# Kernel optimization log

Measured on AMD Instinct MI355X. Metric: run time of the kernel, lower is better.

The kernel has to match this reference:

```python
import jax, jax.numpy as jnp
import numpy as np

B, T, C, H = 2, 2048, 1024, 16
HD = C // H  # head dim = 64


def setup_inputs() -> dict:
    key = jax.random.key(0)
    k1, k2, k3 = jax.random.split(key, 3)
    scale = 0.02
    x = jax.random.normal(k1, (B, T, C), dtype=jnp.float32)
    w_attn = jax.random.normal(k2, (C, 3 * C), dtype=jnp.float32) * scale
    b_attn = jnp.zeros((3 * C,), dtype=jnp.float32)
    w_proj = jax.random.normal(k3, (C, C), dtype=jnp.float32) * scale
    b_proj = jnp.zeros((C,), dtype=jnp.float32)
    return {"x": x, "w_attn": w_attn, "b_attn": b_attn, "w_proj": w_proj, "b_proj": b_proj}


def reference(x, w_attn, b_attn, w_proj, b_proj):
    b, t, c = x.shape
    qkv = x @ w_attn + b_attn  # [B,T,3C]
    q, k, v = jnp.split(qkv, 3, axis=-1)
    # [B,T,C] -> [B,H,T,HD]
    q = q.reshape(b, t, H, HD).transpose(0, 2, 1, 3)
    k = k.reshape(b, t, H, HD).transpose(0, 2, 1, 3)
    v = v.reshape(b, t, H, HD).transpose(0, 2, 1, 3)
    att = jnp.einsum('bhqd,bhkd->bhqk', q, k) * (1.0 / jnp.sqrt(jnp.float32(HD)))
    causal = jnp.tril(jnp.ones((t, t), dtype=bool))  # [T,T]
    att = jnp.where(causal[None, None, :, :], att, jnp.float32(-jnp.inf))
    att = jax.nn.softmax(att, axis=-1)
    y = jnp.einsum('bhqk,bhkd->bhqd', att, v)
    y = y.transpose(0, 2, 1, 3).reshape(b, t, c)
    return y @ w_proj + b_proj
```

## Files before the change

kernel.cpp:

```cpp
#include <hip/hip_runtime.h>


typedef unsigned short u16;
typedef unsigned short u16x8 __attribute__((ext_vector_type(8)));
typedef __bf16 bf16x8 __attribute__((ext_vector_type(8)));
typedef __bf16 bf16x4 __attribute__((ext_vector_type(4)));
typedef float f32x4 __attribute__((ext_vector_type(4)));

#define MFMA16(a, b, c) __builtin_amdgcn_mfma_f32_16x16x32_bf16(a, b, c, 0, 0, 0)

static __device__ __forceinline__ u16 f2b(float f) {
  union { float f; unsigned int i; } x; x.f = f;
  unsigned int r = x.i + 0x7fffu + ((x.i >> 16) & 1u);
  return (u16)(r >> 16);
}
static __device__ __forceinline__ float b2f(u16 u) {
  union { unsigned int i; float f; } x; x.i = ((unsigned int)u) << 16; return x.f;
}

static __device__ __forceinline__ void gload_lds16(const u16* g, u16* l) {
#if defined(__HIP_DEVICE_COMPILE__)
  __builtin_amdgcn_global_load_lds(
      (const __attribute__((address_space(1))) unsigned int*)g,
      (__attribute__((address_space(3))) unsigned int*)l,
      16, 0, 0);
#else
  (void)g; (void)l;
#endif
}

__global__ __launch_bounds__(256) void cast_f32_bf16(
    const float* __restrict__ in, u16* __restrict__ out) {
  int i = (blockIdx.x * 256 + threadIdx.x) * 8;
  float4 a = *(const float4*)&in[i];
  float4 b = *(const float4*)&in[i + 4];
  u16x8 o;
  o[0] = f2b(a.x); o[1] = f2b(a.y); o[2] = f2b(a.z); o[3] = f2b(a.w);
  o[4] = f2b(b.x); o[5] = f2b(b.y); o[6] = f2b(b.z); o[7] = f2b(b.w);
  *(u16x8*)&out[i] = o;
}

__global__ __launch_bounds__(256) void transpose_f32_bf16(
    const float* __restrict__ in, u16* __restrict__ out, int R, int Cc) {
  __shared__ u16 tile[32][33];
  int bx = blockIdx.x, by = blockIdx.y;
  int tx = threadIdx.x, ty = threadIdx.y;
#pragma unroll
  for (int i = 0; i < 4; i++) {
    int r = by * 32 + ty + i * 8;
    int c = bx * 32 + tx;
    tile[ty + i * 8][tx] = f2b(in[r * Cc + c]);
  }
  __syncthreads();
#pragma unroll
  for (int i = 0; i < 4; i++) {
    int r = bx * 32 + ty + i * 8;
    int c = by * 32 + tx;
    out[r * R + c] = tile[tx][ty + i * 8];
  }
}

__global__ __launch_bounds__(256) void transpose_v(
    const u16* __restrict__ in, u16* __restrict__ out) {
  int bh = blockIdx.y;
  int t = blockIdx.x * 128 + (threadIdx.x & 127);
  int dg = (threadIdx.x >> 7) * 32;
  const u16* src = in + (bh * 2048 + t) * 64;
  int p = t & 31;
  int tp = (t & ~31) | ((((p >> 2) & 3) << 3) | ((p >> 4) << 2) | (p & 3));
  u16* dst = out + bh * 64 * 2048 + tp;
#pragma unroll
  for (int i = 0; i < 32; i++) {
    int d = dg + i;
    dst[d * 2048] = src[d];
  }
}

template <int MODE>
__global__ __launch_bounds__(256, 3) void gemm_bt(
    const u16* __restrict__ A, const u16* __restrict__ Bt,
    const float* __restrict__ bias, float* __restrict__ out,
    u16* __restrict__ Qb, u16* __restrict__ Kb, u16* __restrict__ Vb,
    int M, int N, int K) {
  __shared__ u16 lA[128 * 32];
  __shared__ u16 lB[128 * 32];

  const int tid = threadIdx.x;
  const int lane = tid & 63;
  const int w = tid >> 6;
  const int wm = (w >> 1) * 64, wn = (w & 1) * 64;
  const int l15 = lane & 15, quad = lane >> 4;
  const int m0 = blockIdx.y * 128, n0 = blockIdx.x * 128;

  const int srow = lane >> 2;
  const int scol = (lane & 3) * 8;

  f32x4 acc[4][4] = {};

  for (int k0 = 0; k0 < K; k0 += 32) {
    __syncthreads();
#pragma unroll
    for (int h = 0; h < 2; h++) {
      int r = h * 64 + w * 16 + srow;
      gload_lds16(&A[(m0 + r) * K + k0 + scol], &lA[h * 2048 + w * 512 + lane * 8]);
      gload_lds16(&Bt[(n0 + r) * K + k0 + scol], &lB[h * 2048 + w * 512 + lane * 8]);
    }
    __syncthreads();

    bf16x8 af[4], bfr[4];
#pragma unroll
    for (int mi = 0; mi < 4; mi++)
      af[mi] = *(const bf16x8*)&lA[(wm + mi * 16 + l15) * 32 + quad * 8];
#pragma unroll
    for (int ni = 0; ni < 4; ni++)
      bfr[ni] = *(const bf16x8*)&lB[(wn + ni * 16 + l15) * 32 + quad * 8];
#pragma unroll
    for (int mi = 0; mi < 4; mi++)
#pragma unroll
      for (int ni = 0; ni < 4; ni++)
        acc[mi][ni] = MFMA16(af[mi], bfr[ni], acc[mi][ni]);
  }

#pragma unroll
  for (int mi = 0; mi < 4; mi++) {
#pragma unroll
    for (int ni = 0; ni < 4; ni++) {
      int n = n0 + wn + ni * 16 + l15;
      float bv = bias[n];
#pragma unroll
      for (int reg = 0; reg < 4; reg++) {
        int m = m0 + wm + mi * 16 + quad * 4 + reg;
        float v = acc[mi][ni][reg] + bv;
        if (MODE == 1) {
          out[m * N + n] = v;
        } else {
          int which = n >> 10;
          if (which == 1) v *= 0.18033688011112042f;
          int hn = n & 1023;
          int hh = hn >> 6, d = hn & 63;
          int b = m >> 11, t = m & 2047;
          u16* dst = (which == 0) ? Qb : ((which == 1) ? Kb : Vb);
          dst[(((b << 4) + hh) * 2048 + t) * 64 + d] = f2b(v);
        }
      }
    }
  }
}

__global__ __launch_bounds__(256, 4) void attn_split(
    const u16* __restrict__ Qg, const u16* __restrict__ Kg,
    const u16* __restrict__ Vt, u16* __restrict__ Yg,
    u16* __restrict__ Opart, float* __restrict__ lpart) {
  __shared__ u16 lk[2][64 * 64];
  __shared__ u16 lvt[2][64 * 64];

  const int x = blockIdx.x;
  const int bh = blockIdx.y;
  int qt, s, ns;
  if (x < 8)       { qt = x;                s = 0;            ns = 1; }
  else if (x < 24) { int r = x - 8;  qt = 8  + (r >> 1); s = r & 1; ns = 2; }
  else if (x < 48) { int r = x - 24; qt = 16 + r / 3;    s = r % 3; ns = 3; }
  else             { int r = x - 48; qt = 24 + (r >> 2); s = r & 3; ns = 4; }
  const int total = qt + 1;
  const int kts  = (s * total) / ns;
  const int kend = ((s + 1) * total) / ns;

  const int tid = threadIdx.x;
  const int lane = tid & 63;
  const int w = tid >> 6;
  const int l15 = lane & 15, quad = lane >> 4;
  const int qbase = qt * 64;
  const int base = bh * 2048 * 64;
  const int vbase = bh * 64 * 2048;
  const int qloc = w * 16 + l15;
  const int xsw = (l15 & 7) << 3;

  const int sr = tid >> 3;
  const int sc = (tid & 7) * 8;

  const u16* qrow = Qg + base + (qbase + w * 16 + l15) * 64;
  bf16x8 bq0 = *(const bf16x8*)&qrow[quad * 8];
  bf16x8 bq1 = *(const bf16x8*)&qrow[32 + quad * 8];

  u16x8 onesu = {0x3F80, 0x3F80, 0x3F80, 0x3F80, 0x3F80, 0x3F80, 0x3F80, 0x3F80};
  bf16x8 ones = *(const bf16x8*)&onesu;

  const u16* kp = Kg + base;
  const u16* vp = Vt + vbase;

  u16x8 kr[2], vr[2];
  {
    int kvb = kts * 64;
#pragma unroll
    for (int h = 0; h < 2; h++) {
      int r = sr + h * 32;
      kr[h] = *(const u16x8*)&kp[(kvb + r) * 64 + sc];
      vr[h] = *(const u16x8*)&vp[r * 2048 + kvb + sc];
    }
  }

  f32x4 oacc[4] = {};
  f32x4 lacc = {};

  int cur = 0;
  for (int kt = kts; kt < kend; kt++) {
    u16* lkc = lk[cur];
    u16* lvc = lvt[cur];
#pragma unroll
    for (int h = 0; h < 2; h++) {
      int r = sr + h * 32;
      int cs = sc ^ ((r & 7) << 3);
      *(u16x8*)&lkc[r * 64 + cs] = kr[h];
      *(u16x8*)&lvc[r * 64 + cs] = vr[h];
    }
    __syncthreads();
    if (kt + 1 < kend) {
      int kvb = (kt + 1) * 64;
#pragma unroll
      for (int h = 0; h < 2; h++) {
        int r = sr + h * 32;
        kr[h] = *(const u16x8*)&kp[(kvb + r) * 64 + sc];
        vr[h] = *(const u16x8*)&vp[r * 2048 + kvb + sc];
      }
    }

    const bool diag = (kt == qt);

#pragma unroll
    for (int u = 0; u < 2; u++) {
      bf16x8 pa;
#pragma unroll
      for (int half = 0; half < 2; half++) {
        int nt = 2 * u + half;
        const u16* kb = &lkc[(nt * 16 + l15) * 64];
        bf16x8 ak0 = *(const bf16x8*)&kb[(quad * 8) ^ xsw];
        bf16x8 ak1 = *(const bf16x8*)&kb[(32 + quad * 8) ^ xsw];
        f32x4 st = {};
        st = MFMA16(ak0, bq0, st);
        st = MFMA16(ak1, bq1, st);
#pragma unroll
        for (int reg = 0; reg < 4; reg++) {
          float sv = st[reg];
          if (diag && (nt * 16 + quad * 4 + reg) > qloc) sv = -1e30f;
          pa[half * 4 + reg] = (__bf16)__builtin_amdgcn_exp2f(sv);
        }
      }
      lacc = MFMA16(pa, ones, lacc);
#pragma unroll
      for (int dt = 0; dt < 4; dt++) {
        bf16x8 bv = *(const bf16x8*)&lvc[(dt * 16 + l15) * 64 +
                                         ((u * 32 + quad * 8) ^ xsw)];
        oacc[dt] = MFMA16(pa, bv, oacc[dt]);
      }
    }
    cur ^= 1;
  }

  if (ns == 1) {
    const int b = bh >> 4, hh = bh & 15;
    float inv[4];
#pragma unroll
    for (int reg = 0; reg < 4; reg++) inv[reg] = 1.0f / lacc[reg];
#pragma unroll
    for (int dt = 0; dt < 4; dt++)
#pragma unroll
      for (int reg = 0; reg < 4; reg++) {
        int q = qbase + w * 16 + quad * 4 + reg;
        int col = hh * 64 + dt * 16 + l15;
        Yg[(b * 2048 + q) * 1024 + col] = f2b(oacc[dt][reg] * inv[reg]);
      }
  } else {
    const int p = bh * 80 + x;
    u16* op = Opart + p * 4096 + (w * 16) * 64;
#pragma unroll
    for (int dt = 0; dt < 4; dt++)
#pragma unroll
      for (int reg = 0; reg < 4; reg++)
        op[(quad * 4 + reg) * 64 + dt * 16 + l15] = f2b(oacc[dt][reg]);
    if (l15 == 0) {
#pragma unroll
      for (int reg = 0; reg < 4; reg++)
        lpart[p * 64 + w * 16 + quad * 4 + reg] = lacc[reg];
    }
  }
}

__global__ __launch_bounds__(256) void attn_combine(
    const u16* __restrict__ Opart, const float* __restrict__ lpart,
    u16* __restrict__ Yg) {
  const int qt = 8 + blockIdx.x;
  const int bh = blockIdx.y;
  const int tid = threadIdx.x;
  const int row = tid >> 2;
  const int cg = (tid & 3) * 16;
  int xb, ns;
  if (qt < 16)      { xb = 8  + (qt - 8) * 2;  ns = 2; }
  else if (qt < 24) { xb = 24 + (qt - 16) * 3; ns = 3; }
  else              { xb = 48 + (qt - 24) * 4; ns = 4; }

  float acc[16] = {};
  float lsum = 0.f;
  for (int i = 0; i < ns; i++) {
    int p = bh * 80 + xb + i;
    lsum += lpart[p * 64 + row];
    const u16* oprow = Opart + p * 4096 + row * 64 + cg;
    u16x8 a = *(const u16x8*)&oprow[0];
    u16x8 b = *(const u16x8*)&oprow[8];
#pragma unroll
    for (int j = 0; j < 8; j++) { acc[j] += b2f(a[j]); acc[8 + j] += b2f(b[j]); }
  }
  float inv = 1.0f / lsum;
  u16x8 o0, o1;
#pragma unroll
  for (int j = 0; j < 8; j++) { o0[j] = f2b(acc[j] * inv); o1[j] = f2b(acc[8 + j] * inv); }
  const int b = bh >> 4, hh = bh & 15;
  u16* y = Yg + ((long)(b * 2048 + qt * 64 + row)) * 1024 + hh * 64 + cg;
  *(u16x8*)&y[0] = o0;
  *(u16x8*)&y[8] = o1;
}

__global__ __launch_bounds__(256, 4) void attn_kernel(
    const u16* __restrict__ Qg, const u16* __restrict__ Kg,
    const u16* __restrict__ Vt, u16* __restrict__ Yg) {
  __shared__ u16 lk[64 * 64];
  __shared__ u16 lvt[64 * 64];

  const int qt = 31 - blockIdx.x;
  const int bh = blockIdx.y;
  const int tid = threadIdx.x;
  const int lane = tid & 63;
  const int w = tid >> 6;
  const int l15 = lane & 15, quad = lane >> 4;
  const int qbase = qt * 64;
  const int base = bh * 2048 * 64;
  const int vbase = bh * 64 * 2048;
  const int sr = tid >> 3;
  const int sc = (tid & 7) * 8;
  const int xsw = (l15 & 7) << 3;

  const u16* qrow = Qg + base + (qbase + w * 16 + l15) * 64;
  bf16x8 bq0 = *(const bf16x8*)&qrow[quad * 8];
  bf16x8 bq1 = *(const bf16x8*)&qrow[32 + quad * 8];

  u16x8 onesu = {0x3F80, 0x3F80, 0x3F80, 0x3F80, 0x3F80, 0x3F80, 0x3F80, 0x3F80};
  bf16x8 ones = *(const bf16x8*)&onesu;

  const u16* kp = Kg + base;
  const u16* vp = Vt + vbase;

  u16x8 kr[2], vr[2];
#pragma unroll
  for (int h = 0; h < 2; h++) {
    int r = sr + h * 32;
    kr[h] = *(const u16x8*)&kp[r * 64 + sc];
    vr[h] = *(const u16x8*)&vp[r * 2048 + sc];
  }

  f32x4 oacc[4] = {};
  f32x4 lacc = {};

  for (int kt = 0; kt <= qt; kt++) {
    __syncthreads();
#pragma unroll
    for (int h = 0; h < 2; h++) {
      int r = sr + h * 32;
      int cs = sc ^ ((r & 7) << 3);
      *(u16x8*)&lk[r * 64 + cs] = kr[h];
      *(u16x8*)&lvt[r * 64 + cs] = vr[h];
    }
    __syncthreads();
    if (kt < qt) {
      int kvb = (kt + 1) * 64;
#pragma unroll
      for (int h = 0; h < 2; h++) {
        int r = sr + h * 32;
        kr[h] = *(const u16x8*)&kp[(kvb + r) * 64 + sc];
        vr[h] = *(const u16x8*)&vp[r * 2048 + kvb + sc];
      }
    }

    const bool diag = (kt == qt);
    const int qloc = w * 16 + l15;
#pragma unroll
    for (int u = 0; u < 2; u++) {
      bf16x8 pa;
#pragma unroll
      for (int half = 0; half < 2; half++) {
        int nt = 2 * u + half;
        const u16* kb = &lk[(nt * 16 + l15) * 64];
        bf16x8 ak0 = *(const bf16x8*)&kb[(quad * 8) ^ xsw];
        bf16x8 ak1 = *(const bf16x8*)&kb[(32 + quad * 8) ^ xsw];
        f32x4 st = {};
        st = MFMA16(ak0, bq0, st);
        st = MFMA16(ak1, bq1, st);
#pragma unroll
        for (int reg = 0; reg < 4; reg++) {
          float sv = st[reg];
          if (diag && (nt * 16 + quad * 4 + reg) > qloc) sv = -1e30f;
          pa[half * 4 + reg] = (__bf16)__builtin_amdgcn_exp2f(sv);
        }
      }
      lacc = MFMA16(pa, ones, lacc);
#pragma unroll
      for (int dt = 0; dt < 4; dt++) {
        bf16x8 bv = *(const bf16x8*)&lvt[(dt * 16 + l15) * 64 +
                                         ((u * 32 + quad * 8) ^ xsw)];
        oacc[dt] = MFMA16(pa, bv, oacc[dt]);
      }
    }
  }

  const int b = bh >> 4, hh = bh & 15;
  float inv[4];
#pragma unroll
  for (int reg = 0; reg < 4; reg++) inv[reg] = 1.0f / lacc[reg];
#pragma unroll
  for (int dt = 0; dt < 4; dt++)
#pragma unroll
    for (int reg = 0; reg < 4; reg++) {
      int q = qbase + w * 16 + quad * 4 + reg;
      int col = hh * 64 + dt * 16 + l15;
      Yg[(b * 2048 + q) * 1024 + col] = f2b(oacc[dt][reg] * inv[reg]);
    }
}

extern "C" void kernel_launch(void* const* d_in, const int* in_sizes, int n_in,
                              void* d_out, int out_size, void* d_ws, size_t ws_size,
                              hipStream_t stream) {
  const float* x      = (const float*)d_in[0];
  const float* w_attn = (const float*)d_in[1];
  const float* b_attn = (const float*)d_in[2];
  const float* w_proj = (const float*)d_in[3];
  const float* b_proj = (const float*)d_in[4];
  float* out = (float*)d_out;

  char* ws = (char*)d_ws;
  u16* wattnT = (u16*)(ws);
  u16* wprojT = (u16*)(ws + 6291456);
  u16* xb     = (u16*)(ws + 8388608);
  u16* Vt     = xb;
  u16* Qb     = (u16*)(ws + 16777216);
  u16* Kb     = (u16*)(ws + 25165824);
  u16* Vb     = (u16*)(ws + 33554432);
  u16* Yb     = (u16*)(ws + 41943040);
  u16* Opart  = (u16*)(ws + 50331648);
  float* lpart = (float*)(ws + 71303168);

  const bool split = (ws_size >= 71958528ULL);

  cast_f32_bf16<<<2048, 256, 0, stream>>>(x, xb);
  transpose_f32_bf16<<<dim3(96, 32), dim3(32, 8), 0, stream>>>(w_attn, wattnT, 1024, 3072);
  transpose_f32_bf16<<<dim3(32, 32), dim3(32, 8), 0, stream>>>(w_proj, wprojT, 1024, 1024);
  gemm_bt<0><<<dim3(24, 32), 256, 0, stream>>>(xb, wattnT, b_attn, nullptr,
                                               Qb, Kb, Vb, 4096, 3072, 1024);
  transpose_v<<<dim3(16, 32), 256, 0, stream>>>(Vb, Vt);
  if (split) {
    attn_split<<<dim3(80, 32), 256, 0, stream>>>(Qb, Kb, Vt, Yb, Opart, lpart);
    attn_combine<<<dim3(24, 32), 256, 0, stream>>>(Opart, lpart, Yb);
  } else {
    attn_kernel<<<dim3(32, 32), 256, 0, stream>>>(Qb, Kb, Vt, Yb);
  }
  gemm_bt<1><<<dim3(8, 32), 256, 0, stream>>>(Yb, wprojT, b_proj, out,
                                              nullptr, nullptr, nullptr, 4096, 1024, 1024);
}
```

Baseline: 193.8 us.

## Fuse V transpose into QKV GEMM epilogue with swapped MFMA operands and block swizzle

Removes the separate transpose_v kernel and writes V directly in the permuted transposed layout from the QKV GEMM epilogue. For Q/K tiles the MFMA operands are swapped so each lane holds four consecutive head-dim values, allowing vectorized 8-byte stores. A block-index remap spreads tiles across 8 groups, likely to help L2/XCD locality. This saves one kernel launch and a full pass over V, at the cost of a more complex epilogue and a branch inside the K loop.

```diff
diff --git a/kernel.cpp b/kernel.cpp
--- a/kernel.cpp
+++ b/kernel.cpp
@@ -3,6 +3,7 @@
 
 typedef unsigned short u16;
 typedef unsigned short u16x8 __attribute__((ext_vector_type(8)));
+typedef unsigned short u16x4 __attribute__((ext_vector_type(4)));
 typedef __bf16 bf16x8 __attribute__((ext_vector_type(8)));
 typedef __bf16 bf16x4 __attribute__((ext_vector_type(4)));
 typedef float f32x4 __attribute__((ext_vector_type(4)));
@@ -60,27 +61,11 @@
   }
 }
 
-__global__ __launch_bounds__(256) void transpose_v(
-    const u16* __restrict__ in, u16* __restrict__ out) {
-  int bh = blockIdx.y;
-  int t = blockIdx.x * 128 + (threadIdx.x & 127);
-  int dg = (threadIdx.x >> 7) * 32;
-  const u16* src = in + (bh * 2048 + t) * 64;
-  int p = t & 31;
-  int tp = (t & ~31) | ((((p >> 2) & 3) << 3) | ((p >> 4) << 2) | (p & 3));
-  u16* dst = out + bh * 64 * 2048 + tp;
-#pragma unroll
-  for (int i = 0; i < 32; i++) {
-    int d = dg + i;
-    dst[d * 2048] = src[d];
-  }
-}
-
 template <int MODE>
 __global__ __launch_bounds__(256, 3) void gemm_bt(
     const u16* __restrict__ A, const u16* __restrict__ Bt,
     const float* __restrict__ bias, float* __restrict__ out,
-    u16* __restrict__ Qb, u16* __restrict__ Kb, u16* __restrict__ Vb,
+    u16* __restrict__ Qb, u16* __restrict__ Kb, u16* __restrict__ Vtb,
     int M, int N, int K) {
   __shared__ u16 lA[128 * 32];
   __shared__ u16 lB[128 * 32];
@@ -90,7 +75,14 @@
   const int w = tid >> 6;
   const int wm = (w >> 1) * 64, wn = (w & 1) * 64;
   const int l15 = lane & 15, quad = lane >> 4;
-  const int m0 = blockIdx.y * 128, n0 = blockIdx.x * 128;
+
+  const int nx = gridDim.x;
+  const int id = blockIdx.y * nx + blockIdx.x;
+  const int chunk = (nx * gridDim.y) >> 3;
+  const int nid = (id & 7) * chunk + (id >> 3);
+  const int m0 = (nid / nx) * 128, n0 = (nid % nx) * 128;
+
+  const bool swapcd = (MODE == 0) && (n0 < 2048);
 
   const int srow = lane >> 2;
   const int scol = (lane & 3) * 8;
@@ -114,34 +106,76 @@
 #pragma unroll
     for (int ni = 0; ni < 4; ni++)
       bfr[ni] = *(const bf16x8*)&lB[(wn + ni * 16 + l15) * 32 + quad * 8];
-#pragma unroll
-    for (int mi = 0; mi < 4; mi++)
-#pragma unroll
-      for (int ni = 0; ni < 4; ni++)
-        acc[mi][ni] = MFMA16(af[mi], bfr[ni], acc[mi][ni]);
-  }
-
-#pragma unroll
-  for (int mi = 0; mi < 4; mi++) {
-#pragma unroll
-    for (int ni = 0; ni < 4; ni++) {
-      int n = n0 + wn + ni * 16 + l15;
-      float bv = bias[n];
-#pragma unroll
-      for (int reg = 0; reg < 4; reg++) {
-        int m = m0 + wm + mi * 16 + quad * 4 + reg;
-        float v = acc[mi][ni][reg] + bv;
-        if (MODE == 1) {
-          out[m * N + n] = v;
-        } else {
-          int which = n >> 10;
-          if (which == 1) v *= 0.18033688011112042f;
-          int hn = n & 1023;
-          int hh = hn >> 6, d = hn & 63;
-          int b = m >> 11, t = m & 2047;
-          u16* dst = (which == 0) ? Qb : ((which == 1) ? Kb : Vb);
-          dst[(((b << 4) + hh) * 2048 + t) * 64 + d] = f2b(v);
+    if (swapcd) {
+#pragma unroll
+      for (int mi = 0; mi < 4; mi++)
+#pragma unroll
+        for (int ni = 0; ni < 4; ni++)
+          acc[mi][ni] = MFMA16(bfr[ni], af[mi], acc[mi][ni]);
+    } else {
+#pragma unroll
+      for (int mi = 0; mi < 4; mi++)
+#pragma unroll
+        for (int ni = 0; ni < 4; ni++)
+          acc[mi][ni] = MFMA16(af[mi], bfr[ni], acc[mi][ni]);
+    }
+  }
+
+  if (MODE == 1) {
+#pragma unroll
+    for (int mi = 0; mi < 4; mi++) {
+#pragma unroll
+      for (int ni = 0; ni < 4; ni++) {
+        int n = n0 + wn + ni * 16 + l15;
+        float bv = bias[n];
+#pragma unroll
+        for (int reg = 0; reg < 4; reg++) {
+          int m = m0 + wm + mi * 16 + quad * 4 + reg;
+          out[m * N + n] = acc[mi][ni][reg] + bv;
         }
+      }
+    }
+  } else if (n0 < 2048) {
+    const int which = n0 >> 10;
+    u16* dst = which ? Kb : Qb;
+    const float scale = which ? 0.18033688011112042f : 1.0f;
+    const int b = m0 >> 11;
+    const int hh = ((n0 & 1023) + wn) >> 6;
+    const int tbase = (m0 & 2047) + wm + l15;
+#pragma unroll
+    for (int mi = 0; mi < 4; mi++) {
+      u16* drow = dst + (((b << 4) + hh) * 2048 + tbase + mi * 16) * 64;
+#pragma unroll
+      for (int ni = 0; ni < 4; ni++) {
+        int d0 = ni * 16 + quad * 4;
+        float4 bv4 = *(const float4*)&bias[n0 + wn + d0];
+        u16x4 o;
+        o[0] = f2b((acc[mi][ni][0] + bv4.x) * scale);
+        o[1] = f2b((acc[mi][ni][1] + bv4.y) * scale);
+        o[2] = f2b((acc[mi][ni][2] + bv4.z) * scale);
+        o[3] = f2b((acc[mi][ni][3] + bv4.w) * scale);
+        *(u16x4*)&drow[d0] = o;
+      }
+    }
+  } else {
+    const int b = m0 >> 11;
+    const int hh = ((n0 & 1023) + wn) >> 6;
+    const int bh = (b << 4) + hh;
+    const u16* unused = A; (void)unused;
+#pragma unroll
+    for (int mi = 0; mi < 4; mi++) {
+      int t32 = (m0 & 2047) + wm + (mi >> 1) * 32;
+      int tp0 = quad * 8 + (mi & 1) * 4;
+#pragma unroll
+      for (int ni = 0; ni < 4; ni++) {
+        int d = ni * 16 + l15;
+        float bv = bias[n0 + wn + d];
+        u16x4 o;
+        o[0] = f2b(acc[mi][ni][0] + bv);
+        o[1] = f2b(acc[mi][ni][1] + bv);
+        o[2] = f2b(acc[mi][ni][2] + bv);
+        o[3] = f2b(acc[mi][ni][3] + bv);
+        *(u16x4*)&Vtb[(bh * 64 + d) * 2048 + t32 + tp0] = o;
       }
     }
   }
@@ -438,10 +472,9 @@
   u16* wattnT = (u16*)(ws);
   u16* wprojT = (u16*)(ws + 6291456);
   u16* xb     = (u16*)(ws + 8388608);
-  u16* Vt     = xb;
   u16* Qb     = (u16*)(ws + 16777216);
   u16* Kb     = (u16*)(ws + 25165824);
-  u16* Vb     = (u16*)(ws + 33554432);
+  u16* Vt     = (u16*)(ws + 33554432);
   u16* Yb     = (u16*)(ws + 41943040);
   u16* Opart  = (u16*)(ws + 50331648);
   float* lpart = (float*)(ws + 71303168);
@@ -452,8 +485,7 @@
   transpose_f32_bf16<<<dim3(96, 32), dim3(32, 8), 0, stream>>>(w_attn, wattnT, 1024, 3072);
   transpose_f32_bf16<<<dim3(32, 32), dim3(32, 8), 0, stream>>>(w_proj, wprojT, 1024, 1024);
   gemm_bt<0><<<dim3(24, 32), 256, 0, stream>>>(xb, wattnT, b_attn, nullptr,
-                                               Qb, Kb, Vb, 4096, 3072, 1024);
-  transpose_v<<<dim3(16, 32), 256, 0, stream>>>(Vb, Vt);
+                                               Qb, Kb, Vt, 4096, 3072, 1024);
   if (split) {
     attn_split<<<dim3(80, 32), 256, 0, stream>>>(Qb, Kb, Vt, Yb, Opart, lpart);
     attn_combine<<<dim3(24, 32), 256, 0, stream>>>(Opart, lpart, Yb);
```

After: 193.4 us. Within noise of the previous version (-0.2%).
